# Optimization experiments

Hardware: AMD Instinct MI355X
Metric: run time of the kernel (lower is better)

## Reference

```python
import jax, jax.numpy as jnp
import numpy as np

WIDTHS = [2, 3, 5, 8, 13, 21, 34, 55, 89, 26]  # ragged one-hot feature widths, sum = 256
NSEG = len(WIDTHS)
B, IN = 8192, 256
LAYOUT = [1024, 1024, 1024, 256]
EPS = 1e-5  # BatchNorm1d default eps
TAU = 1.0


def setup_inputs() -> dict:
    key = jax.random.key(0)
    ks = iter(jax.random.split(key, 64))
    inp = {"x": jax.random.normal(next(ks), (B, IN), jnp.float32)}
    prev = IN
    for i, fc in enumerate(LAYOUT):
        inp[f"W{i}"] = jax.random.normal(next(ks), (fc, prev), jnp.float32) / np.float32(np.sqrt(prev))
        inp[f"b{i}"] = 0.01 * jax.random.normal(next(ks), (fc,), jnp.float32)
        if i + 1 < len(LAYOUT):  # Residual blocks carry BatchNorm params (eval mode)
            inp[f"g{i}"] = 1.0 + 0.1 * jax.random.normal(next(ks), (fc,), jnp.float32)
            inp[f"be{i}"] = 0.1 * jax.random.normal(next(ks), (fc,), jnp.float32)
            inp[f"rm{i}"] = 0.1 * jax.random.normal(next(ks), (fc,), jnp.float32)
            inp[f"rv{i}"] = 0.75 + 0.5 * jax.random.uniform(next(ks), (fc,), dtype=jnp.float32)
        prev += fc
    inp["seg_ids"] = jnp.asarray(np.repeat(np.arange(NSEG), WIDTHS), jnp.int32)  # [256]
    return inp


def _residual(x, W, b, g, be, rm, rv):
    # Linear -> eval-mode BatchNorm1d -> ReLU -> concat([out, input])
    h = x @ W.T + b
    h = (h - rm) * (g * jax.lax.rsqrt(rv + EPS)) + be
    return jnp.concatenate([jax.nn.relu(h), x], axis=1)


def _segment_softmax(x, seg_ids):
    # Fused segmented softmax over ragged feature groups (replaces per-feature Python loop)
    xt = x.T / TAU                                            # [F, B]
    m = jax.ops.segment_max(xt, seg_ids, num_segments=NSEG)   # [NSEG, B]
    e = jnp.exp(xt - m[seg_ids])
    s = jax.ops.segment_sum(e, seg_ids, num_segments=NSEG)
    return (e / s[seg_ids]).T                                 # [B, F]


def reference(x, W0, b0, g0, be0, rm0, rv0, W1, b1, g1, be1, rm1, rv1,
              W2, b2, g2, be2, rm2, rv2, W3, b3, seg_ids):
    h = _residual(x, W0, b0, g0, be0, rm0, rv0)   # [B, 1280]
    h = _residual(h, W1, b1, g1, be1, rm1, rv1)   # [B, 2304]
    h = _residual(h, W2, b2, g2, be2, rm2, rv2)   # [B, 3328]
    h = h @ W3.T + b3                              # [B, 256]
    return _segment_softmax(h, seg_ids)
```

## Files before the change

### kernel.cpp

```cpp
#include <hip/hip_runtime.h>
#include <hip/hip_fp16.h>


#define LDH 3328
#define NROWS 8192

typedef _Float16 f16x8 __attribute__((ext_vector_type(8)));
typedef _Float16 f16x4 __attribute__((ext_vector_type(4)));
typedef float f32x4 __attribute__((ext_vector_type(4)));

__constant__ int c_bnd[11] = {0, 2, 5, 10, 18, 31, 52, 86, 141, 230, 256};

__device__ __forceinline__ void async_cp16(const _Float16* g, _Float16* l) {
  __builtin_amdgcn_global_load_lds(
      (__attribute__((address_space(1))) void*)g,
      (__attribute__((address_space(3))) void*)l, 16, 0, 0);
}

__device__ __forceinline__ _Float16 f2h(float f) { return (_Float16)f; }

__global__ void prep_kernel(const float* __restrict__ s0,
                            const float* __restrict__ s1,
                            const float* __restrict__ s2,
                            const float* __restrict__ s3,
                            const float* __restrict__ x,
                            const float* __restrict__ b3,
                            _Float16* __restrict__ d0,
                            _Float16* __restrict__ d1,
                            _Float16* __restrict__ d2,
                            _Float16* __restrict__ d3,
                            _Float16* __restrict__ H, float* __restrict__ out,
                            int n0, int n1, int n2, int n3, int n4, int n5) {
  int i = blockIdx.x * blockDim.x + threadIdx.x;
  if (i >= n5) return;
  if (i >= n4) {
    const int j = i - n4;
    const int c = (j & 63) * 4;
    *(float4*)&out[(size_t)j * 4] = *(const float4*)&b3[c];
    return;
  }
  if (i >= n3) {
    const int j = i - n3;
    const int row = j >> 6;
    const int c = (j & 63) * 4;
    const float4 v = *(const float4*)&x[(size_t)j * 4];
    f16x4 h = {f2h(v.x), f2h(v.y), f2h(v.z), f2h(v.w)};
    *(f16x4*)&H[(size_t)row * LDH + 3072 + c] = h;
    return;
  }
  const float* s;
  _Float16* d;
  if (i < n0) {
    s = s0; d = d0;
  } else if (i < n1) {
    s = s1 - (size_t)n0 * 4; d = d1 - (size_t)n0 * 4;
  } else if (i < n2) {
    s = s2 - (size_t)n1 * 4; d = d2 - (size_t)n1 * 4;
  } else {
    s = s3 - (size_t)n2 * 4; d = d3 - (size_t)n2 * 4;
  }
  const float4 v = *(const float4*)&s[(size_t)i * 4];
  f16x4 h = {f2h(v.x), f2h(v.y), f2h(v.z), f2h(v.w)};
  *(f16x4*)&d[(size_t)i * 4] = h;
}

__launch_bounds__(256, 2) __global__
void gemm_bn_kernel(const _Float16* __restrict__ A, int K,
                    const _Float16* __restrict__ W,
                    const float* __restrict__ bias,
                    const float* __restrict__ g, const float* __restrict__ be,
                    const float* __restrict__ rm,
                    const float* __restrict__ rv, _Float16* __restrict__ outH,
                    int outOff) {
  __shared__ _Float16 Alds[128 * 128];
  __shared__ _Float16 Blds[128 * 128];

  const int tid = threadIdx.x;
  const int lane = tid & 63;
  const int wave = tid >> 6;
  const int wr = wave >> 1;
  const int wc = wave & 1;
  const int row0 = blockIdx.x * 128;
  const int col0 = blockIdx.y * 128;
  const int lr4 = lane >> 4;
  const int sl = lane & 15;
  const int fr = lane & 15;
  const int q = lane >> 4;

  f32x4 acc[4][4] = {};

  for (int k0 = 0; k0 < K; k0 += 128) {
    __syncthreads();
#pragma unroll
    for (int it = 0; it < 8; ++it) {
      const int j = it * 4 + wave;
      const int r = j * 4 + lr4;
      const int gc = sl ^ (r & 7);
      async_cp16(A + (size_t)(row0 + r) * LDH + k0 + gc * 8, &Alds[j * 512]);
      async_cp16(W + (size_t)(col0 + r) * K + k0 + gc * 8, &Blds[j * 512]);
    }
    __syncthreads();

#pragma unroll
    for (int kq = 0; kq < 4; ++kq) {
      f16x8 av[4], bv[4];
#pragma unroll
      for (int t = 0; t < 4; ++t) {
        const int ra = wr * 64 + t * 16 + fr;
        av[t] =
            *(const f16x8*)&Alds[ra * 128 + (((kq * 4 + q) ^ (ra & 7)) * 8)];
        const int rb = wc * 64 + t * 16 + fr;
        bv[t] =
            *(const f16x8*)&Blds[rb * 128 + (((kq * 4 + q) ^ (rb & 7)) * 8)];
      }
#pragma unroll
      for (int tm = 0; tm < 4; ++tm)
#pragma unroll
        for (int tn = 0; tn < 4; ++tn)
          acc[tm][tn] = __builtin_amdgcn_mfma_f32_16x16x32_f16(
              av[tm], bv[tn], acc[tm][tn], 0, 0, 0);
    }
  }

#pragma unroll
  for (int tn = 0; tn < 4; ++tn) {
    const int n = col0 + wc * 64 + tn * 16 + fr;
    const float alpha = g[n] * rsqrtf(rv[n] + 1e-5f);
    const float beta = (bias[n] - rm[n]) * alpha + be[n];
#pragma unroll
    for (int tm = 0; tm < 4; ++tm) {
      const int rbase = row0 + wr * 64 + tm * 16 + q * 4;
#pragma unroll
      for (int r = 0; r < 4; ++r) {
        float v = acc[tm][tn][r] * alpha + beta;
        v = fmaxf(v, 0.0f);
        outH[(size_t)(rbase + r) * LDH + outOff + n] = f2h(v);
      }
    }
  }
}

__launch_bounds__(256, 4) __global__
void gemm_out_kernel(const _Float16* __restrict__ A,
                     const _Float16* __restrict__ W,
                     float* __restrict__ out) {
  __shared__ _Float16 Alds[128 * 64];
  __shared__ _Float16 Blds[128 * 64];

  const int tid = threadIdx.x;
  const int lane = tid & 63;
  const int wave = tid >> 6;
  const int wr = wave >> 1;
  const int wc = wave & 1;
  const int row0 = blockIdx.x * 128;
  const int cb = blockIdx.y & 1;
  const int ks = blockIdx.y >> 1;
  const int col0 = cb * 128;
  const int k0b = ks * 832;
  const int k0e = k0b + 832;
  const int lr = lane >> 3;
  const int ls = lane & 7;
  const int lc = ls ^ lr;
  const int fr = lane & 15;
  const int q = lane >> 4;
  const int K = 3328;

  f32x4 acc[4][4] = {};

  for (int k0 = k0b; k0 < k0e; k0 += 64) {
    __syncthreads();
#pragma unroll
    for (int it = 0; it < 4; ++it) {
      const int rl = it * 32 + wave * 8;
      async_cp16(A + (size_t)(row0 + rl + lr) * LDH + k0 + lc * 8,
                 &Alds[rl * 64]);
      async_cp16(W + (size_t)(col0 + rl + lr) * K + k0 + lc * 8,
                 &Blds[rl * 64]);
    }
    __syncthreads();

#pragma unroll
    for (int kq = 0; kq < 2; ++kq) {
      f16x8 av[4], bv[4];
#pragma unroll
      for (int t = 0; t < 4; ++t) {
        const int ra = wr * 64 + t * 16 + fr;
        av[t] = *(const f16x8*)&Alds[ra * 64 + (((q + 4 * kq) ^ (ra & 7)) * 8)];
        const int rb = wc * 64 + t * 16 + fr;
        bv[t] = *(const f16x8*)&Blds[rb * 64 + (((q + 4 * kq) ^ (rb & 7)) * 8)];
      }
#pragma unroll
      for (int tm = 0; tm < 4; ++tm)
#pragma unroll
        for (int tn = 0; tn < 4; ++tn)
          acc[tm][tn] = __builtin_amdgcn_mfma_f32_16x16x32_f16(
              av[tm], bv[tn], acc[tm][tn], 0, 0, 0);
    }
  }

#pragma unroll
  for (int tn = 0; tn < 4; ++tn) {
    const int n = col0 + wc * 64 + tn * 16 + fr;
#pragma unroll
    for (int tm = 0; tm < 4; ++tm) {
      const int rbase = row0 + wr * 64 + tm * 16 + q * 4;
#pragma unroll
      for (int r = 0; r < 4; ++r)
        atomicAdd(&out[(size_t)(rbase + r) * 256 + n], acc[tm][tn][r]);
    }
  }
}

__global__ void segsoftmax_kernel(float* __restrict__ out,
                                  const int* __restrict__ segids) {
  __shared__ float vals[4][256];
  __shared__ float red[4][10];
  const int w = threadIdx.x >> 6;
  const int l = threadIdx.x & 63;
  const int row = blockIdx.x * 4 + w;
  float4 v = *(float4*)&out[(size_t)row * 256 + l * 4];
  *(float4*)&vals[w][l * 4] = v;
  __syncthreads();
  if (l < 10) {
    float m = -1e30f;
    for (int j = c_bnd[l]; j < c_bnd[l + 1]; ++j) m = fmaxf(m, vals[w][j]);
    red[w][l] = m;
  }
  __syncthreads();
  const int4 s4 = *(const int4*)&segids[l * 4];
  float4 e;
  e.x = expf(v.x - red[w][s4.x]);
  e.y = expf(v.y - red[w][s4.y]);
  e.z = expf(v.z - red[w][s4.z]);
  e.w = expf(v.w - red[w][s4.w]);
  *(float4*)&vals[w][l * 4] = e;
  __syncthreads();
  if (l < 10) {
    float s = 0.0f;
    for (int j = c_bnd[l]; j < c_bnd[l + 1]; ++j) s += vals[w][j];
    red[w][l] = s;
  }
  __syncthreads();
  float4 o;
  o.x = e.x / red[w][s4.x];
  o.y = e.y / red[w][s4.y];
  o.z = e.z / red[w][s4.z];
  o.w = e.w / red[w][s4.w];
  *(float4*)&out[(size_t)row * 256 + l * 4] = o;
}

extern "C" void kernel_launch(void* const* d_in, const int* in_sizes, int n_in,
                              void* d_out, int out_size, void* d_ws,
                              size_t ws_size, hipStream_t stream) {
  const float* x = (const float*)d_in[0];
  const float* W0 = (const float*)d_in[1];
  const float* b0 = (const float*)d_in[2];
  const float* g0 = (const float*)d_in[3];
  const float* be0 = (const float*)d_in[4];
  const float* rm0 = (const float*)d_in[5];
  const float* rv0 = (const float*)d_in[6];
  const float* W1 = (const float*)d_in[7];
  const float* b1 = (const float*)d_in[8];
  const float* g1 = (const float*)d_in[9];
  const float* be1 = (const float*)d_in[10];
  const float* rm1 = (const float*)d_in[11];
  const float* rv1 = (const float*)d_in[12];
  const float* W2 = (const float*)d_in[13];
  const float* b2 = (const float*)d_in[14];
  const float* g2 = (const float*)d_in[15];
  const float* be2 = (const float*)d_in[16];
  const float* rm2 = (const float*)d_in[17];
  const float* rv2 = (const float*)d_in[18];
  const float* W3 = (const float*)d_in[19];
  const float* b3 = (const float*)d_in[20];
  const int* seg = (const int*)d_in[21];
  float* out = (float*)d_out;

  _Float16* H = (_Float16*)d_ws;
  size_t off = (size_t)NROWS * LDH;
  _Float16* Wh0 = H + off; off += 1024 * 256;
  _Float16* Wh1 = H + off; off += 1024 * 1280;
  _Float16* Wh2 = H + off; off += 1024 * 2304;
  _Float16* Wh3 = H + off;

  const int n0 = 65536, n1 = n0 + 327680, n2 = n1 + 589824, n3 = n2 + 212992;
  const int n4 = n3 + 524288, n5 = n4 + 524288;
  prep_kernel<<<(n5 + 255) / 256, 256, 0, stream>>>(
      W0, W1, W2, W3, x, b3, Wh0, Wh1, Wh2, Wh3, H, out, n0, n1, n2, n3, n4,
      n5);

  dim3 blk(256);
  gemm_bn_kernel<<<dim3(64, 8), blk, 0, stream>>>(
      H + 3072, 256, Wh0, b0, g0, be0, rm0, rv0, H, 2048);
  gemm_bn_kernel<<<dim3(64, 8), blk, 0, stream>>>(
      H + 2048, 1280, Wh1, b1, g1, be1, rm1, rv1, H, 1024);
  gemm_bn_kernel<<<dim3(64, 8), blk, 0, stream>>>(
      H + 1024, 2304, Wh2, b2, g2, be2, rm2, rv2, H, 0);
  gemm_out_kernel<<<dim3(64, 8), blk, 0, stream>>>(H, Wh3, out);
  segsoftmax_kernel<<<2048, 256, 0, stream>>>(out, seg);
}
```

Before: 247.2 us.

## Switch GEMMs to 32x32x16 MFMA and shrink BN GEMM K-tile to 64

Both GEMM kernels now use the 32x32x16 f16 MFMA with 2x2 accumulator tiles per wave instead of a 4x4 grid of 16x16x32 MFMAs. This halves the number of LDS fragment reads per k-step. The BN GEMM also drops its K tile from 128 to 64, halving LDS use, and raises launch bounds to 4 blocks per CU to increase occupancy. In exchange there are twice as many barrier-separated load phases per K, and the epilogue store pattern becomes more scattered.

Measured after the change: 265.1 us. 7.3% more time.

```diff
diff --git a/kernel.cpp b/kernel.cpp
--- a/kernel.cpp
+++ b/kernel.cpp
@@ -7,7 +7,7 @@
 
 typedef _Float16 f16x8 __attribute__((ext_vector_type(8)));
 typedef _Float16 f16x4 __attribute__((ext_vector_type(4)));
-typedef float f32x4 __attribute__((ext_vector_type(4)));
+typedef float f32x16 __attribute__((ext_vector_type(16)));
 
 __constant__ int c_bnd[11] = {0, 2, 5, 10, 18, 31, 52, 86, 141, 230, 256};
 
@@ -64,7 +64,7 @@
   *(f16x4*)&d[(size_t)i * 4] = h;
 }
 
-__launch_bounds__(256, 2) __global__
+__launch_bounds__(256, 4) __global__
 void gemm_bn_kernel(const _Float16* __restrict__ A, int K,
                     const _Float16* __restrict__ W,
                     const float* __restrict__ bias,
@@ -72,8 +72,8 @@
                     const float* __restrict__ rm,
                     const float* __restrict__ rv, _Float16* __restrict__ outH,
                     int outOff) {
-  __shared__ _Float16 Alds[128 * 128];
-  __shared__ _Float16 Blds[128 * 128];
+  __shared__ _Float16 Alds[128 * 64];
+  __shared__ _Float16 Blds[128 * 64];
 
   const int tid = threadIdx.x;
   const int lane = tid & 63;
@@ -82,59 +82,61 @@
   const int wc = wave & 1;
   const int row0 = blockIdx.x * 128;
   const int col0 = blockIdx.y * 128;
-  const int lr4 = lane >> 4;
-  const int sl = lane & 15;
-  const int fr = lane & 15;
-  const int q = lane >> 4;
-
-  f32x4 acc[4][4] = {};
-
-  for (int k0 = 0; k0 < K; k0 += 128) {
+  const int lr = lane >> 3;
+  const int ls = lane & 7;
+  const int lc = ls ^ lr;
+  const int fm = lane & 31;
+  const int hk = lane >> 5;
+
+  f32x16 acc[2][2] = {};
+
+  for (int k0 = 0; k0 < K; k0 += 64) {
     __syncthreads();
 #pragma unroll
-    for (int it = 0; it < 8; ++it) {
-      const int j = it * 4 + wave;
-      const int r = j * 4 + lr4;
-      const int gc = sl ^ (r & 7);
-      async_cp16(A + (size_t)(row0 + r) * LDH + k0 + gc * 8, &Alds[j * 512]);
-      async_cp16(W + (size_t)(col0 + r) * K + k0 + gc * 8, &Blds[j * 512]);
+    for (int it = 0; it < 4; ++it) {
+      const int rl = it * 32 + wave * 8;
+      async_cp16(A + (size_t)(row0 + rl + lr) * LDH + k0 + lc * 8,
+                 &Alds[rl * 64]);
+      async_cp16(W + (size_t)(col0 + rl + lr) * K + k0 + lc * 8,
+                 &Blds[rl * 64]);
     }
     __syncthreads();
 
 #pragma unroll
-    for (int kq = 0; kq < 4; ++kq) {
-      f16x8 av[4], bv[4];
-#pragma unroll
-      for (int t = 0; t < 4; ++t) {
-        const int ra = wr * 64 + t * 16 + fr;
+    for (int ks = 0; ks < 4; ++ks) {
+      f16x8 av[2], bv[2];
+#pragma unroll
+      for (int t = 0; t < 2; ++t) {
+        const int ra = wr * 64 + t * 32 + fm;
         av[t] =
-            *(const f16x8*)&Alds[ra * 128 + (((kq * 4 + q) ^ (ra & 7)) * 8)];
-        const int rb = wc * 64 + t * 16 + fr;
+            *(const f16x8*)&Alds[ra * 64 + (((ks * 2 + hk) ^ (ra & 7)) * 8)];
+        const int rb = wc * 64 + t * 32 + fm;
         bv[t] =
-            *(const f16x8*)&Blds[rb * 128 + (((kq * 4 + q) ^ (rb & 7)) * 8)];
+            *(const f16x8*)&Blds[rb * 64 + (((ks * 2 + hk) ^ (rb & 7)) * 8)];
       }
 #pragma unroll
-      for (int tm = 0; tm < 4; ++tm)
-#pragma unroll
-        for (int tn = 0; tn < 4; ++tn)
-          acc[tm][tn] = __builtin_amdgcn_mfma_f32_16x16x32_f16(
+      for (int tm = 0; tm < 2; ++tm)
+#pragma unroll
+        for (int tn = 0; tn < 2; ++tn)
+          acc[tm][tn] = __builtin_amdgcn_mfma_f32_32x32x16_f16(
               av[tm], bv[tn], acc[tm][tn], 0, 0, 0);
     }
   }
 
 #pragma unroll
-  for (int tn = 0; tn < 4; ++tn) {
-    const int n = col0 + wc * 64 + tn * 16 + fr;
+  for (int tn = 0; tn < 2; ++tn) {
+    const int n = col0 + wc * 64 + tn * 32 + fm;
     const float alpha = g[n] * rsqrtf(rv[n] + 1e-5f);
     const float beta = (bias[n] - rm[n]) * alpha + be[n];
 #pragma unroll
-    for (int tm = 0; tm < 4; ++tm) {
-      const int rbase = row0 + wr * 64 + tm * 16 + q * 4;
-#pragma unroll
-      for (int r = 0; r < 4; ++r) {
-        float v = acc[tm][tn][r] * alpha + beta;
+    for (int tm = 0; tm < 2; ++tm) {
+      const int rbase = row0 + wr * 64 + tm * 32 + 4 * hk;
+#pragma unroll
+      for (int reg = 0; reg < 16; ++reg) {
+        const int row = rbase + (reg & 3) + 8 * (reg >> 2);
+        float v = acc[tm][tn][reg] * alpha + beta;
         v = fmaxf(v, 0.0f);
-        outH[(size_t)(rbase + r) * LDH + outOff + n] = f2h(v);
+        outH[(size_t)row * LDH + outOff + n] = f2h(v);
       }
     }
   }
@@ -154,18 +156,18 @@
   const int wc = wave & 1;
   const int row0 = blockIdx.x * 128;
   const int cb = blockIdx.y & 1;
-  const int ks = blockIdx.y >> 1;
+  const int ksl = blockIdx.y >> 1;
   const int col0 = cb * 128;
-  const int k0b = ks * 832;
+  const int k0b = ksl * 832;
   const int k0e = k0b + 832;
   const int lr = lane >> 3;
   const int ls = lane & 7;
   const int lc = ls ^ lr;
-  const int fr = lane & 15;
-  const int q = lane >> 4;
+  const int fm = lane & 31;
+  const int hk = lane >> 5;
   const int K = 3328;
 
-  f32x4 acc[4][4] = {};
+  f32x16 acc[2][2] = {};
 
   for (int k0 = k0b; k0 < k0e; k0 += 64) {
     __syncthreads();
@@ -180,33 +182,37 @@
     __syncthreads();
 
 #pragma unroll
-    for (int kq = 0; kq < 2; ++kq) {
-      f16x8 av[4], bv[4];
-#pragma unroll
-      for (int t = 0; t < 4; ++t) {
-        const int ra = wr * 64 + t * 16 + fr;
-        av[t] = *(const f16x8*)&Alds[ra * 64 + (((q + 4 * kq) ^ (ra & 7)) * 8)];
-        const int rb = wc * 64 + t * 16 + fr;
-        bv[t] = *(const f16x8*)&Blds[rb * 64 + (((q + 4 * kq) ^ (rb & 7)) * 8)];
+    for (int ks = 0; ks < 4; ++ks) {
+      f16x8 av[2], bv[2];
+#pragma unroll
+      for (int t = 0; t < 2; ++t) {
+        const int ra = wr * 64 + t * 32 + fm;
+        av[t] =
+            *(const f16x8*)&Alds[ra * 64 + (((ks * 2 + hk) ^ (ra & 7)) * 8)];
+        const int rb = wc * 64 + t * 32 + fm;
+        bv[t] =
+            *(const f16x8*)&Blds[rb * 64 + (((ks * 2 + hk) ^ (rb & 7)) * 8)];
       }
 #pragma unroll
-      for (int tm = 0; tm < 4; ++tm)
-#pragma unroll
-        for (int tn = 0; tn < 4; ++tn)
-          acc[tm][tn] = __builtin_amdgcn_mfma_f32_16x16x32_f16(
+      for (int tm = 0; tm < 2; ++tm)
+#pragma unroll
+        for (int tn = 0; tn < 2; ++tn)
+          acc[tm][tn] = __builtin_amdgcn_mfma_f32_32x32x16_f16(
               av[tm], bv[tn], acc[tm][tn], 0, 0, 0);
     }
   }
 
 #pragma unroll
-  for (int tn = 0; tn < 4; ++tn) {
-    const int n = col0 + wc * 64 + tn * 16 + fr;
-#pragma unroll
-    for (int tm = 0; tm < 4; ++tm) {
-      const int rbase = row0 + wr * 64 + tm * 16 + q * 4;
-#pragma unroll
-      for (int r = 0; r < 4; ++r)
-        atomicAdd(&out[(size_t)(rbase + r) * 256 + n], acc[tm][tn][r]);
+  for (int tn = 0; tn < 2; ++tn) {
+    const int n = col0 + wc * 64 + tn * 32 + fm;
+#pragma unroll
+    for (int tm = 0; tm < 2; ++tm) {
+      const int rbase = row0 + wr * 64 + tm * 32 + 4 * hk;
+#pragma unroll
+      for (int reg = 0; reg < 16; ++reg) {
+        const int row = rbase + (reg & 3) + 8 * (reg >> 2);
+        atomicAdd(&out[(size_t)row * 256 + n], acc[tm][tn][reg]);
+      }
     }
   }
 }
```

## Fuse fp32-to-fp16 prep into first layer GEMM and halve K-tile

Applied to the files above, without the earlier changes.

Removes the separate prep kernel. A new first-layer kernel reads fp32 x and W0 directly, converts them to fp16 while staging into LDS, writes the x copy into the residual buffer, and then converts the remaining weights and initialises the output bias in a grid-stride tail. The gemm_bn kernel's K-tile shrinks from 128 to 64, halving LDS use so launch bounds can rise to 4 blocks per SM for more occupancy. The aim is to save one launch and a pass over memory, at the cost of synchronous, non-async loads in layer 0, extra work appended to that kernel, and twice as many barriers per K in the GEMMs.

Result: slower. 253.6 us (+2.6%).

```diff
diff --git a/kernel.cpp b/kernel.cpp
--- a/kernel.cpp
+++ b/kernel.cpp
@@ -19,52 +19,119 @@
 
 __device__ __forceinline__ _Float16 f2h(float f) { return (_Float16)f; }
 
-__global__ void prep_kernel(const float* __restrict__ s0,
-                            const float* __restrict__ s1,
-                            const float* __restrict__ s2,
-                            const float* __restrict__ s3,
-                            const float* __restrict__ x,
-                            const float* __restrict__ b3,
-                            _Float16* __restrict__ d0,
-                            _Float16* __restrict__ d1,
-                            _Float16* __restrict__ d2,
-                            _Float16* __restrict__ d3,
-                            _Float16* __restrict__ H, float* __restrict__ out,
-                            int n0, int n1, int n2, int n3, int n4, int n5) {
-  int i = blockIdx.x * blockDim.x + threadIdx.x;
-  if (i >= n5) return;
-  if (i >= n4) {
-    const int j = i - n4;
-    const int c = (j & 63) * 4;
-    *(float4*)&out[(size_t)j * 4] = *(const float4*)&b3[c];
-    return;
-  }
-  if (i >= n3) {
-    const int j = i - n3;
-    const int row = j >> 6;
-    const int c = (j & 63) * 4;
-    const float4 v = *(const float4*)&x[(size_t)j * 4];
-    f16x4 h = {f2h(v.x), f2h(v.y), f2h(v.z), f2h(v.w)};
-    *(f16x4*)&H[(size_t)row * LDH + 3072 + c] = h;
-    return;
-  }
-  const float* s;
-  _Float16* d;
-  if (i < n0) {
-    s = s0; d = d0;
-  } else if (i < n1) {
-    s = s1 - (size_t)n0 * 4; d = d1 - (size_t)n0 * 4;
-  } else if (i < n2) {
-    s = s2 - (size_t)n1 * 4; d = d2 - (size_t)n1 * 4;
-  } else {
-    s = s3 - (size_t)n2 * 4; d = d3 - (size_t)n2 * 4;
-  }
-  const float4 v = *(const float4*)&s[(size_t)i * 4];
-  f16x4 h = {f2h(v.x), f2h(v.y), f2h(v.z), f2h(v.w)};
-  *(f16x4*)&d[(size_t)i * 4] = h;
-}
-
-__launch_bounds__(256, 2) __global__
+__device__ __forceinline__ f16x8 cvt8(const float* p) {
+  const float4 a = *(const float4*)p;
+  const float4 b = *(const float4*)(p + 4);
+  f16x8 h = {f2h(a.x), f2h(a.y), f2h(a.z), f2h(a.w),
+             f2h(b.x), f2h(b.y), f2h(b.z), f2h(b.w)};
+  return h;
+}
+
+__launch_bounds__(256, 4) __global__
+void l0_kernel(const float* __restrict__ x, const float* __restrict__ W0f,
+               const float* __restrict__ bias, const float* __restrict__ g,
+               const float* __restrict__ be, const float* __restrict__ rm,
+               const float* __restrict__ rv, const float* __restrict__ W1f,
+               const float* __restrict__ W2f, const float* __restrict__ W3f,
+               const float* __restrict__ b3, _Float16* __restrict__ H,
+               _Float16* __restrict__ Wh1, _Float16* __restrict__ Wh2,
+               _Float16* __restrict__ Wh3, float* __restrict__ out) {
+  __shared__ _Float16 Alds[128 * 64];
+  __shared__ _Float16 Blds[128 * 64];
+
+  const int tid = threadIdx.x;
+  const int lane = tid & 63;
+  const int wave = tid >> 6;
+  const int wr = wave >> 1;
+  const int wc = wave & 1;
+  const int row0 = blockIdx.x * 128;
+  const int col0 = blockIdx.y * 128;
+  const int sr = tid >> 3;
+  const int sl = tid & 7;
+  const int fr = lane & 15;
+  const int q = lane >> 4;
+  const bool wthru = (blockIdx.y == 0);
+
+  f32x4 acc[4][4] = {};
+
+#pragma unroll 1
+  for (int k0 = 0; k0 < 256; k0 += 64) {
+    __syncthreads();
+#pragma unroll
+    for (int it = 0; it < 4; ++it) {
+      const int r = it * 32 + sr;
+      const int gc = sl ^ (r & 7);
+      const f16x8 ah = cvt8(&x[(size_t)(row0 + r) * 256 + k0 + gc * 8]);
+      *(f16x8*)&Alds[r * 64 + sl * 8] = ah;
+      if (wthru)
+        *(f16x8*)&H[(size_t)(row0 + r) * LDH + 3072 + k0 + gc * 8] = ah;
+      const f16x8 bh = cvt8(&W0f[(size_t)(col0 + r) * 256 + k0 + gc * 8]);
+      *(f16x8*)&Blds[r * 64 + sl * 8] = bh;
+    }
+    __syncthreads();
+
+#pragma unroll
+    for (int kq = 0; kq < 2; ++kq) {
+      f16x8 av[4], bv[4];
+#pragma unroll
+      for (int t = 0; t < 4; ++t) {
+        const int ra = wr * 64 + t * 16 + fr;
+        av[t] = *(const f16x8*)&Alds[ra * 64 + (((q + 4 * kq) ^ (ra & 7)) * 8)];
+        const int rb = wc * 64 + t * 16 + fr;
+        bv[t] = *(const f16x8*)&Blds[rb * 64 + (((q + 4 * kq) ^ (rb & 7)) * 8)];
+      }
+#pragma unroll
+      for (int tm = 0; tm < 4; ++tm)
+#pragma unroll
+        for (int tn = 0; tn < 4; ++tn)
+          acc[tm][tn] = __builtin_amdgcn_mfma_f32_16x16x32_f16(
+              av[tm], bv[tn], acc[tm][tn], 0, 0, 0);
+    }
+  }
+
+#pragma unroll
+  for (int tn = 0; tn < 4; ++tn) {
+    const int n = col0 + wc * 64 + tn * 16 + fr;
+    const float alpha = g[n] * rsqrtf(rv[n] + 1e-5f);
+    const float beta = (bias[n] - rm[n]) * alpha + be[n];
+#pragma unroll
+    for (int tm = 0; tm < 4; ++tm) {
+      const int rbase = row0 + wr * 64 + tm * 16 + q * 4;
+#pragma unroll
+      for (int r = 0; r < 4; ++r) {
+        float v = acc[tm][tn][r] * alpha + beta;
+        v = fmaxf(v, 0.0f);
+        H[(size_t)(rbase + r) * LDH + 2048 + n] = f2h(v);
+      }
+    }
+  }
+
+  const int c1 = 327680, c2 = c1 + 589824, c3 = c2 + 212992;
+  const int c4 = c3 + 524288;
+  const int bid = blockIdx.y * 64 + blockIdx.x;
+  for (int i = bid * 256 + tid; i < c4; i += 512 * 256) {
+    if (i < c3) {
+      const float* s;
+      _Float16* d;
+      int j;
+      if (i < c1) {
+        s = W1f; d = Wh1; j = i;
+      } else if (i < c2) {
+        s = W2f; d = Wh2; j = i - c1;
+      } else {
+        s = W3f; d = Wh3; j = i - c2;
+      }
+      const float4 v = *(const float4*)&s[(size_t)j * 4];
+      f16x4 h = {f2h(v.x), f2h(v.y), f2h(v.z), f2h(v.w)};
+      *(f16x4*)&d[(size_t)j * 4] = h;
+    } else {
+      const int j = i - c3;
+      *(float4*)&out[(size_t)j * 4] = *(const float4*)&b3[(j & 63) * 4];
+    }
+  }
+}
+
+__launch_bounds__(256, 4) __global__
 void gemm_bn_kernel(const _Float16* __restrict__ A, int K,
                     const _Float16* __restrict__ W,
                     const float* __restrict__ bias,
@@ -72,8 +139,8 @@
                     const float* __restrict__ rm,
                     const float* __restrict__ rv, _Float16* __restrict__ outH,
                     int outOff) {
-  __shared__ _Float16 Alds[128 * 128];
-  __shared__ _Float16 Blds[128 * 128];
+  __shared__ _Float16 Alds[128 * 64];
+  __shared__ _Float16 Blds[128 * 64];
 
   const int tid = threadIdx.x;
   const int lane = tid & 63;
@@ -82,36 +149,35 @@
   const int wc = wave & 1;
   const int row0 = blockIdx.x * 128;
   const int col0 = blockIdx.y * 128;
-  const int lr4 = lane >> 4;
-  const int sl = lane & 15;
+  const int lr = lane >> 3;
+  const int ls = lane & 7;
+  const int lc = ls ^ lr;
   const int fr = lane & 15;
   const int q = lane >> 4;
 
   f32x4 acc[4][4] = {};
 
-  for (int k0 = 0; k0 < K; k0 += 128) {
-    __syncthreads();
-#pragma unroll
-    for (int it = 0; it < 8; ++it) {
-      const int j = it * 4 + wave;
-      const int r = j * 4 + lr4;
-      const int gc = sl ^ (r & 7);
-      async_cp16(A + (size_t)(row0 + r) * LDH + k0 + gc * 8, &Alds[j * 512]);
-      async_cp16(W + (size_t)(col0 + r) * K + k0 + gc * 8, &Blds[j * 512]);
-    }
-    __syncthreads();
-
-#pragma unroll
-    for (int kq = 0; kq < 4; ++kq) {
+  for (int k0 = 0; k0 < K; k0 += 64) {
+    __syncthreads();
+#pragma unroll
+    for (int it = 0; it < 4; ++it) {
+      const int rl = it * 32 + wave * 8;
+      async_cp16(A + (size_t)(row0 + rl + lr) * LDH + k0 + lc * 8,
+                 &Alds[rl * 64]);
+      async_cp16(W + (size_t)(col0 + rl + lr) * K + k0 + lc * 8,
+                 &Blds[rl * 64]);
+    }
+    __syncthreads();
+
+#pragma unroll
+    for (int kq = 0; kq < 2; ++kq) {
       f16x8 av[4], bv[4];
 #pragma unroll
       for (int t = 0; t < 4; ++t) {
         const int ra = wr * 64 + t * 16 + fr;
-        av[t] =
-            *(const f16x8*)&Alds[ra * 128 + (((kq * 4 + q) ^ (ra & 7)) * 8)];
+        av[t] = *(const f16x8*)&Alds[ra * 64 + (((q + 4 * kq) ^ (ra & 7)) * 8)];
         const int rb = wc * 64 + t * 16 + fr;
-        bv[t] =
-            *(const f16x8*)&Blds[rb * 128 + (((kq * 4 + q) ^ (rb & 7)) * 8)];
+        bv[t] = *(const f16x8*)&Blds[rb * 64 + (((q + 4 * kq) ^ (rb & 7)) * 8)];
       }
 #pragma unroll
       for (int tm = 0; tm < 4; ++tm)
@@ -278,20 +344,13 @@
 
   _Float16* H = (_Float16*)d_ws;
   size_t off = (size_t)NROWS * LDH;
-  _Float16* Wh0 = H + off; off += 1024 * 256;
   _Float16* Wh1 = H + off; off += 1024 * 1280;
   _Float16* Wh2 = H + off; off += 1024 * 2304;
   _Float16* Wh3 = H + off;
 
-  const int n0 = 65536, n1 = n0 + 327680, n2 = n1 + 589824, n3 = n2 + 212992;
-  const int n4 = n3 + 524288, n5 = n4 + 524288;
-  prep_kernel<<<(n5 + 255) / 256, 256, 0, stream>>>(
-      W0, W1, W2, W3, x, b3, Wh0, Wh1, Wh2, Wh3, H, out, n0, n1, n2, n3, n4,
-      n5);
-
   dim3 blk(256);
-  gemm_bn_kernel<<<dim3(64, 8), blk, 0, stream>>>(
-      H + 3072, 256, Wh0, b0, g0, be0, rm0, rv0, H, 2048);
+  l0_kernel<<<dim3(64, 8), blk, 0, stream>>>(
+      x, W0, b0, g0, be0, rm0, rv0, W1, W2, W3, b3, H, Wh1, Wh2, Wh3, out);
   gemm_bn_kernel<<<dim3(64, 8), blk, 0, stream>>>(
       H + 2048, 1280, Wh1, b1, g1, be1, rm1, rv1, H, 1024);
   gemm_bn_kernel<<<dim3(64, 8), blk, 0, stream>>>(
```

## Use 512-thread blocks with a 64-wide K tile in the BN GEMM kernel

Applied to the files above, without the earlier changes.

The BN GEMM kernel now runs with 8 waves per block instead of 4, so each wave computes a 64x32 sub-tile. The K step drops from 128 to 64, which halves LDS per block to 32 KB and allows more resident blocks per CU. This is meant to raise occupancy and latency hiding, at the cost of twice as many barrier-separated K iterations and less register-level reuse per wave. The output GEMM kernel keeps its own 256-thread launch.

Measured after the change: 249.8 us. No clear change (+1.1%).

```diff
diff --git a/kernel.cpp b/kernel.cpp
--- a/kernel.cpp
+++ b/kernel.cpp
@@ -64,7 +64,7 @@
   *(f16x4*)&d[(size_t)i * 4] = h;
 }
 
-__launch_bounds__(256, 2) __global__
+__launch_bounds__(512, 4) __global__
 void gemm_bn_kernel(const _Float16* __restrict__ A, int K,
                     const _Float16* __restrict__ W,
                     const float* __restrict__ bias,
@@ -72,59 +72,61 @@
                     const float* __restrict__ rm,
                     const float* __restrict__ rv, _Float16* __restrict__ outH,
                     int outOff) {
-  __shared__ _Float16 Alds[128 * 128];
-  __shared__ _Float16 Blds[128 * 128];
+  __shared__ _Float16 Alds[128 * 64];
+  __shared__ _Float16 Blds[128 * 64];
 
   const int tid = threadIdx.x;
   const int lane = tid & 63;
   const int wave = tid >> 6;
-  const int wr = wave >> 1;
-  const int wc = wave & 1;
+  const int wr = wave >> 2;
+  const int wcq = wave & 3;
   const int row0 = blockIdx.x * 128;
   const int col0 = blockIdx.y * 128;
-  const int lr4 = lane >> 4;
-  const int sl = lane & 15;
+  const int lr = lane >> 3;
+  const int ls = lane & 7;
+  const int lc = ls ^ lr;
   const int fr = lane & 15;
   const int q = lane >> 4;
 
-  f32x4 acc[4][4] = {};
-
-  for (int k0 = 0; k0 < K; k0 += 128) {
+  f32x4 acc[4][2] = {};
+
+  for (int k0 = 0; k0 < K; k0 += 64) {
     __syncthreads();
 #pragma unroll
-    for (int it = 0; it < 8; ++it) {
-      const int j = it * 4 + wave;
-      const int r = j * 4 + lr4;
-      const int gc = sl ^ (r & 7);
-      async_cp16(A + (size_t)(row0 + r) * LDH + k0 + gc * 8, &Alds[j * 512]);
-      async_cp16(W + (size_t)(col0 + r) * K + k0 + gc * 8, &Blds[j * 512]);
+    for (int it = 0; it < 2; ++it) {
+      const int rl = (it * 8 + wave) * 8;
+      async_cp16(A + (size_t)(row0 + rl + lr) * LDH + k0 + lc * 8,
+                 &Alds[rl * 64]);
+      async_cp16(W + (size_t)(col0 + rl + lr) * K + k0 + lc * 8,
+                 &Blds[rl * 64]);
     }
     __syncthreads();
 
 #pragma unroll
-    for (int kq = 0; kq < 4; ++kq) {
-      f16x8 av[4], bv[4];
+    for (int kq = 0; kq < 2; ++kq) {
+      f16x8 av[4], bv[2];
 #pragma unroll
       for (int t = 0; t < 4; ++t) {
         const int ra = wr * 64 + t * 16 + fr;
-        av[t] =
-            *(const f16x8*)&Alds[ra * 128 + (((kq * 4 + q) ^ (ra & 7)) * 8)];
-        const int rb = wc * 64 + t * 16 + fr;
-        bv[t] =
-            *(const f16x8*)&Blds[rb * 128 + (((kq * 4 + q) ^ (rb & 7)) * 8)];
+        av[t] = *(const f16x8*)&Alds[ra * 64 + (((q + 4 * kq) ^ (ra & 7)) * 8)];
       }
 #pragma unroll
+      for (int t = 0; t < 2; ++t) {
+        const int rb = wcq * 32 + t * 16 + fr;
+        bv[t] = *(const f16x8*)&Blds[rb * 64 + (((q + 4 * kq) ^ (rb & 7)) * 8)];
+      }
+#pragma unroll
       for (int tm = 0; tm < 4; ++tm)
 #pragma unroll
-        for (int tn = 0; tn < 4; ++tn)
+        for (int tn = 0; tn < 2; ++tn)
           acc[tm][tn] = __builtin_amdgcn_mfma_f32_16x16x32_f16(
               av[tm], bv[tn], acc[tm][tn], 0, 0, 0);
     }
   }
 
 #pragma unroll
-  for (int tn = 0; tn < 4; ++tn) {
-    const int n = col0 + wc * 64 + tn * 16 + fr;
+  for (int tn = 0; tn < 2; ++tn) {
+    const int n = col0 + wcq * 32 + tn * 16 + fr;
     const float alpha = g[n] * rsqrtf(rv[n] + 1e-5f);
     const float beta = (bias[n] - rm[n]) * alpha + be[n];
 #pragma unroll
@@ -289,13 +291,13 @@
       W0, W1, W2, W3, x, b3, Wh0, Wh1, Wh2, Wh3, H, out, n0, n1, n2, n3, n4,
       n5);
 
-  dim3 blk(256);
+  dim3 blk(512);
   gemm_bn_kernel<<<dim3(64, 8), blk, 0, stream>>>(
       H + 3072, 256, Wh0, b0, g0, be0, rm0, rv0, H, 2048);
   gemm_bn_kernel<<<dim3(64, 8), blk, 0, stream>>>(
       H + 2048, 1280, Wh1, b1, g1, be1, rm1, rv1, H, 1024);
   gemm_bn_kernel<<<dim3(64, 8), blk, 0, stream>>>(
       H + 1024, 2304, Wh2, b2, g2, be2, rm2, rv2, H, 0);
-  gemm_out_kernel<<<dim3(64, 8), blk, 0, stream>>>(H, Wh3, out);
+  gemm_out_kernel<<<dim3(64, 8), dim3(256), 0, stream>>>(H, Wh3, out);
   segsoftmax_kernel<<<2048, 256, 0, stream>>>(out, seg);
 }
```
